# Kernel optimization log

Hardware: AMD Instinct MI355X
Metric: run time of the kernel (lower is better)

## Reference

```python
import jax, jax.numpy as jnp
import numpy as np

HEAD = 8
ATT = 32  # hard-coded att_num in the module
NEG_INF = -jnp.inf


def setup_inputs() -> dict:
    key0 = jax.random.key(0)
    ks = jax.random.split(key0, 12)
    B, N, Din, Dout = 8, 2048, 256, 256
    W = HEAD * ATT  # 256
    s_in = 1.0 / np.sqrt(Din)
    s_w = 1.0 / np.sqrt(W)
    return {
        "query": jax.random.normal(ks[0], (B, N, Din), jnp.float32),
        "key": jax.random.normal(ks[1], (B, N, Din), jnp.float32),
        "value": jax.random.normal(ks[2], (B, N, Din), jnp.float32),
        # torch.nn.Linear convention: W [out, in], y = x @ W.T + b
        "Wq": jax.random.normal(ks[3], (W, Din), jnp.float32) * s_in,
        "bq": jax.random.normal(ks[4], (W,), jnp.float32) * s_in,
        "Wk": jax.random.normal(ks[5], (W, Din), jnp.float32) * s_in,
        "bk": jax.random.normal(ks[6], (W,), jnp.float32) * s_in,
        "Wv": jax.random.normal(ks[7], (W, Din), jnp.float32) * s_in,
        "bv": jax.random.normal(ks[8], (W,), jnp.float32) * s_in,
        "Wo": jax.random.normal(ks[9], (Dout, W), jnp.float32) * s_w,
        "bo": jax.random.normal(ks[10], (Dout,), jnp.float32) * s_w,
    }


def _split_heads(x, b):
    # [b, n, head*att] -> view(b, n, head, att).permute(2,0,1,3) -> [head*b, n, att]
    n = x.shape[1]
    return x.reshape(b, n, HEAD, ATT).transpose(2, 0, 1, 3).reshape(HEAD * b, n, ATT)


def reference(query, key, value, Wq, bq, Wk, bk, Wv, bv, Wo, bo):
    b = query.shape[0]
    q = _split_heads(query @ Wq.T + bq, b)   # [head*b, nq, att]
    k = _split_heads(key @ Wk.T + bk, b)     # [head*b, nk, att]
    v = _split_heads(value @ Wv.T + bv, b)   # [head*b, nk, att]

    att = jnp.einsum('bmd,bnd->bmn', q, k)   # [head*b, nq, nk]
    nq, nk = att.shape[-2], att.shape[-1]
    causal = jnp.tril(jnp.ones((nq, nk), dtype=bool))
    att = jnp.where(causal, att, NEG_INF)
    att = jax.nn.softmax(att / jnp.sqrt(jnp.float32(ATT)), axis=-1)

    out = jnp.einsum('bmn,bnd->bmd', att, v)  # [head*b, nq, att]
    # view(head, b, nq, att).permute(1,2,0,3) -> [b, nq, head*att]
    out = out.reshape(HEAD, b, nq, ATT).transpose(1, 2, 0, 3).reshape(b, nq, HEAD * ATT)
    return out @ Wo.T + bo
```

## Files before the change

### kernel.cpp

```cpp
#include <hip/hip_runtime.h>
#include <hip/hip_bf16.h>
#include <stdint.h>

typedef __bf16 bf16_t;
typedef __bf16 bf16x4 __attribute__((ext_vector_type(4)));
typedef __bf16 bf16x8 __attribute__((ext_vector_type(8)));
typedef float f32x4 __attribute__((ext_vector_type(4)));
typedef __attribute__((address_space(3))) bf16_t* ldsp;

#define HEADS 8
#define ATTD 32
#define NBATCH 8
#define SEQ 2048
#define DIN 256
#define WDIM 256
#define MTOT (NBATCH*SEQ)
#define HBSZ ((size_t)MTOT*WDIM)
#define SCALE_L2E 0.25503322964704155f

#define EXP2R __builtin_amdgcn_exp2f

__device__ __forceinline__ uint32_t cvtpk(float a, float b) {
    uint32_t r;
    asm("v_cvt_pk_bf16_f32 %0, %1, %2" : "=v"(r) : "v"(a), "v"(b));
    return r;
}

template<int MODE>
__global__ __launch_bounds__(256) void gemm_kernel(
    const void* __restrict__ X0, const void* __restrict__ X1,
    const void* __restrict__ X2,
    const float* __restrict__ W0, const float* __restrict__ W1,
    const float* __restrict__ W2,
    const float* __restrict__ b0, const float* __restrict__ b1,
    const float* __restrict__ b2, void* __restrict__ outbase)
{
    __shared__ bf16_t As[128*64];
    __shared__ bf16_t Bs[128*64];

    const int tid = threadIdx.x;
    const int z   = blockIdx.z;
    const int m0  = blockIdx.y * 128;
    const int n0  = blockIdx.x * 128;
    const void*  Xin  = (z == 0) ? X0 : (z == 1) ? X1 : X2;
    const float* Wf   = (z == 0) ? W0 : (z == 1) ? W1 : W2;
    const float* bias = (z == 0) ? b0 : (z == 1) ? b1 : b2;

    const int wv = tid >> 6, ln = tid & 63, g = ln >> 4, l15 = ln & 15;
    const int wm = wv >> 1, wn = wv & 1;

    f32x4 acc[4][4];
#pragma unroll
    for (int i = 0; i < 4; ++i)
#pragma unroll
        for (int j = 0; j < 4; ++j) acc[i][j] = (f32x4){0.f,0.f,0.f,0.f};

    for (int kt = 0; kt < DIN/64; ++kt) {
        if (kt) __syncthreads();
#pragma unroll
        for (int iss = 0; iss < 4; ++iss) {
            int chunk = iss*256 + tid;
            int row = chunk >> 3, c8 = (chunk & 7) * 8;
            union { bf16_t h[8]; bf16x8 v; } av, bvv;
            if (MODE == 0) {
                const float* A = (const float*)Xin;
                float4 a0 = *(const float4*)(A + (size_t)(m0+row)*DIN + kt*64 + c8);
                float4 a1 = *(const float4*)(A + (size_t)(m0+row)*DIN + kt*64 + c8 + 4);
                av.h[0]=(bf16_t)a0.x; av.h[1]=(bf16_t)a0.y; av.h[2]=(bf16_t)a0.z; av.h[3]=(bf16_t)a0.w;
                av.h[4]=(bf16_t)a1.x; av.h[5]=(bf16_t)a1.y; av.h[6]=(bf16_t)a1.z; av.h[7]=(bf16_t)a1.w;
            } else {
                av.v = *(const bf16x8*)((const bf16_t*)Xin + (size_t)(m0+row)*DIN + kt*64 + c8);
            }
            float4 w0 = *(const float4*)(Wf + (size_t)(n0+row)*DIN + kt*64 + c8);
            float4 w1 = *(const float4*)(Wf + (size_t)(n0+row)*DIN + kt*64 + c8 + 4);
            bvv.h[0]=(bf16_t)w0.x; bvv.h[1]=(bf16_t)w0.y; bvv.h[2]=(bf16_t)w0.z; bvv.h[3]=(bf16_t)w0.w;
            bvv.h[4]=(bf16_t)w1.x; bvv.h[5]=(bf16_t)w1.y; bvv.h[6]=(bf16_t)w1.z; bvv.h[7]=(bf16_t)w1.w;
            *(bf16x8*)(As + chunk*8) = av.v;
            *(bf16x8*)(Bs + chunk*8) = bvv.v;
        }
        __syncthreads();
#pragma unroll
        for (int kk = 0; kk < 2; ++kk) {
            bf16x8 af[4], bfr[4];
#pragma unroll
            for (int i = 0; i < 4; ++i)
                af[i] = *(const bf16x8*)(As + (wm*64 + i*16 + l15)*64 + kk*32 + g*8);
#pragma unroll
            for (int j = 0; j < 4; ++j)
                bfr[j] = *(const bf16x8*)(Bs + (wn*64 + j*16 + l15)*64 + kk*32 + g*8);
#pragma unroll
            for (int i = 0; i < 4; ++i)
#pragma unroll
                for (int j = 0; j < 4; ++j)
                    acc[i][j] = __builtin_amdgcn_mfma_f32_16x16x32_bf16(
                        af[i], bfr[j], acc[i][j], 0, 0, 0);
        }
    }

    if (MODE == 0) {
        const int mrow   = m0 + wm*64 + g*4;
        const int ohbase = (n0 >> 5) + wn*2;
        bf16_t* out = (bf16_t*)outbase + (size_t)z * HBSZ;
        const float sc = (z == 0) ? SCALE_L2E : 1.0f;
#pragma unroll
        for (int j = 0; j < 4; ++j) {
            const int oh = ohbase + (j >> 1);
            const int ol = (j & 1)*16 + l15;
            bf16_t* p = out + ((size_t)oh*MTOT + mrow)*ATTD + ol;
            const float bb = bias[(oh << 5) | ol];
#pragma unroll
            for (int i = 0; i < 4; ++i)
#pragma unroll
                for (int r = 0; r < 4; ++r)
                    p[i*16*ATTD + r*ATTD] = (bf16_t)((acc[i][j][r] + bb) * sc);
        }
    } else {
        const int mrow = m0 + wm*64 + g*4;
        const int ocol = n0 + wn*64 + l15;
        float* out = (float*)outbase;
        float bb[4];
#pragma unroll
        for (int j = 0; j < 4; ++j) bb[j] = bias[ocol + j*16];
#pragma unroll
        for (int i = 0; i < 4; ++i) {
            float* p = out + (size_t)(mrow + i*16)*WDIM + ocol;
#pragma unroll
            for (int j = 0; j < 4; ++j)
#pragma unroll
                for (int r = 0; r < 4; ++r)
                    p[r*WDIM + j*16] = acc[i][j][r] + bb[j];
        }
    }
}

__global__ __launch_bounds__(512) void attn_kernel(
    const bf16_t* __restrict__ Qh, const bf16_t* __restrict__ Kh,
    const bf16_t* __restrict__ Vh, bf16_t* __restrict__ ATTo)
{
    __shared__ __align__(1024) bf16_t Ks[2][2][64*40];
    __shared__ __align__(1024) bf16_t Vsub[2][2][2048];

    const int qtx = blockIdx.x;
    const int bh  = blockIdx.y;
    const int hh = bh >> 3, bb = bh & 7;
    const int tid = threadIdx.x;
    const int wv = tid >> 6, ln = tid & 63, g = ln >> 4, l15 = ln & 15;
    const int grp = wv >> 2;
    const int wvi = wv & 3;
    const int t256 = tid & 255;

    const int kr = t256 >> 2, kc = (t256 & 3) * 8;
    const int vdst = ((kr >> 2) * 2 + ((t256 & 3) >> 1)) * 64 + (kr & 3) * 16 + (t256 & 1) * 8;
    const f32x4 zero4 = {0.f,0.f,0.f,0.f};
    const size_t bhs = (size_t)bh * SEQ;

    float* scr = (float*)&Ks[0][0][0];

    bf16x8 ones;
#pragma unroll
    for (int e = 0; e < 8; ++e) ones[e] = (bf16_t)1.0f;

    for (int half = 0; half < 2; ++half) {
        const int qt = half ? (31 - qtx) : qtx;
        const int n0 = qt * 64;
        const int nIter = (qt >> 1) + 1;
        const int q = n0 + wvi*16 + l15;
        const bf16x8 qfrag = *(const bf16x8*)(Qh + (bhs + q)*ATTD + g*8);
        f32x4 o0 = zero4, o1 = zero4, lsum = zero4;
        float m = -1e30f;

        {
            bf16x8 k0 = *(const bf16x8*)(Kh + (bhs + grp*64 + kr)*ATTD + kc);
            bf16x8 v0 = *(const bf16x8*)(Vh + (bhs + grp*64 + kr)*ATTD + kc);
            __syncthreads();
            *(bf16x8*)(&Ks[grp][0][kr*40 + kc]) = k0;
            *(bf16x8*)(&Vsub[grp][0][vdst]) = v0;
        }

        const bf16_t* kpref = Kh + (bhs + (grp+2)*64 + kr)*ATTD + kc;
        const bf16_t* vpref = Vh + (bhs + (grp+2)*64 + kr)*ATTD + kc;

        for (int t = 0; t < nIter; ++t) {
            const int cur = t & 1;
            const int myT = 2*t + grp;
            bf16x8 kreg = *(const bf16x8*)kpref; kpref += 128*ATTD;
            bf16x8 vreg = *(const bf16x8*)vpref; vpref += 128*ATTD;
            __syncthreads();

            if (myT <= qt) {
                f32x4 s[4];
#pragma unroll
                for (int c = 0; c < 4; ++c) {
                    bf16x8 kf = *(const bf16x8*)(&Ks[grp][cur][(c*16 + l15)*40 + g*8]);
                    s[c] = __builtin_amdgcn_mfma_f32_16x16x32_bf16(kf, qfrag, zero4, 0, 0, 0);
                }
                if (myT == qt) {
#pragma unroll
                    for (int c = 0; c < 4; ++c)
#pragma unroll
                        for (int r = 0; r < 4; ++r)
                            if (c*16 + g*4 + r > wvi*16 + l15) s[c][r] = -1e30f;
                }
                float t0 = fmaxf(fmaxf(s[0][0], s[0][1]), s[0][2]);
                float t1 = fmaxf(fmaxf(s[0][3], s[1][0]), s[1][1]);
                float t2 = fmaxf(fmaxf(s[1][2], s[1][3]), s[2][0]);
                float t3 = fmaxf(fmaxf(s[2][1], s[2][2]), s[2][3]);
                float t4 = fmaxf(fmaxf(s[3][0], s[3][1]), s[3][2]);
                float pmax = fmaxf(fmaxf(fmaxf(t0, t1), fmaxf(t2, t3)),
                                   fmaxf(t4, s[3][3]));
                pmax = fmaxf(pmax, __shfl_xor(pmax, 16));
                pmax = fmaxf(pmax, __shfl_xor(pmax, 32));
                if (!__all(pmax <= m)) {
                    const float mnew = fmaxf(m, pmax);
                    const float alpha = EXP2R(m - mnew);
                    m = mnew;
                    lsum[0] *= alpha;
#pragma unroll
                    for (int r = 0; r < 4; ++r) { o0[r] *= alpha; o1[r] *= alpha; }
                }
                union { uint32_t u[4]; bf16x8 v; } pb0, pb1;
                pb0.u[0] = cvtpk(EXP2R(s[0][0]-m), EXP2R(s[0][1]-m));
                pb0.u[1] = cvtpk(EXP2R(s[0][2]-m), EXP2R(s[0][3]-m));
                pb0.u[2] = cvtpk(EXP2R(s[1][0]-m), EXP2R(s[1][1]-m));
                pb0.u[3] = cvtpk(EXP2R(s[1][2]-m), EXP2R(s[1][3]-m));
                pb1.u[0] = cvtpk(EXP2R(s[2][0]-m), EXP2R(s[2][1]-m));
                pb1.u[1] = cvtpk(EXP2R(s[2][2]-m), EXP2R(s[2][3]-m));
                pb1.u[2] = cvtpk(EXP2R(s[3][0]-m), EXP2R(s[3][1]-m));
                pb1.u[3] = cvtpk(EXP2R(s[3][2]-m), EXP2R(s[3][3]-m));
                ldsp va = (ldsp)&Vsub[grp][cur][0] + g*128 + l15*4;
                bf16x4 t00, t01, t02, t03, t10, t11, t12, t13;
                asm volatile("ds_read_b64_tr_b16 %0, %1 offset:0"    : "=v"(t00) : "v"(va));
                asm volatile("ds_read_b64_tr_b16 %0, %1 offset:1024" : "=v"(t01) : "v"(va));
                asm volatile("ds_read_b64_tr_b16 %0, %1 offset:2048" : "=v"(t02) : "v"(va));
                asm volatile("ds_read_b64_tr_b16 %0, %1 offset:3072" : "=v"(t03) : "v"(va));
                asm volatile("ds_read_b64_tr_b16 %0, %1 offset:128"  : "=v"(t10) : "v"(va));
                asm volatile("ds_read_b64_tr_b16 %0, %1 offset:1152" : "=v"(t11) : "v"(va));
                asm volatile("ds_read_b64_tr_b16 %0, %1 offset:2176" : "=v"(t12) : "v"(va));
                asm volatile("ds_read_b64_tr_b16 %0, %1 offset:3200" : "=v"(t13) : "v"(va));
                asm volatile("s_waitcnt lgkmcnt(0)" ::: "memory");
                __builtin_amdgcn_sched_barrier(0);
                o0 = __builtin_amdgcn_mfma_f32_16x16x32_bf16(
                    __builtin_shufflevector(t00, t01, 0,1,2,3,4,5,6,7), pb0.v, o0, 0,0,0);
                o0 = __builtin_amdgcn_mfma_f32_16x16x32_bf16(
                    __builtin_shufflevector(t02, t03, 0,1,2,3,4,5,6,7), pb1.v, o0, 0,0,0);
                o1 = __builtin_amdgcn_mfma_f32_16x16x32_bf16(
                    __builtin_shufflevector(t10, t11, 0,1,2,3,4,5,6,7), pb0.v, o1, 0,0,0);
                o1 = __builtin_amdgcn_mfma_f32_16x16x32_bf16(
                    __builtin_shufflevector(t12, t13, 0,1,2,3,4,5,6,7), pb1.v, o1, 0,0,0);
                lsum = __builtin_amdgcn_mfma_f32_16x16x32_bf16(ones, pb0.v, lsum, 0,0,0);
                lsum = __builtin_amdgcn_mfma_f32_16x16x32_bf16(ones, pb1.v, lsum, 0,0,0);
            }

            *(bf16x8*)(&Ks[grp][cur^1][kr*40 + kc]) = kreg;
            *(bf16x8*)(&Vsub[grp][cur^1][vdst]) = vreg;
        }

        __syncthreads();
        const int sidx = (wvi*64 + ln)*10;
        if (grp == 1) {
            scr[sidx]   = m;
            scr[sidx+1] = lsum[0];
#pragma unroll
            for (int r = 0; r < 4; ++r) { scr[sidx+2+r] = o0[r]; scr[sidx+6+r] = o1[r]; }
        }
        __syncthreads();
        if (grp == 0) {
            const float mB = scr[sidx], lB = scr[sidx+1];
            const float mM = fmaxf(m, mB);
            const float aA = EXP2R(m - mM), aB = EXP2R(mB - mM);
            const float inv = 1.f / (lsum[0]*aA + lB*aB);
            union { bf16_t h[4]; uint2 u; } w0, w1;
#pragma unroll
            for (int r = 0; r < 4; ++r) {
                w0.h[r] = (bf16_t)((o0[r]*aA + scr[sidx+2+r]*aB) * inv);
                w1.h[r] = (bf16_t)((o1[r]*aA + scr[sidx+6+r]*aB) * inv);
            }
            const size_t base = ((size_t)bb*SEQ + q)*WDIM + hh*ATTD;
            *(uint2*)(ATTo + base + g*4)      = w0.u;
            *(uint2*)(ATTo + base + 16 + g*4) = w1.u;
        }
    }
}

extern "C" void kernel_launch(void* const* d_in, const int* in_sizes, int n_in,
                              void* d_out, int out_size, void* d_ws, size_t ws_size,
                              hipStream_t stream) {
    const float* q_in = (const float*)d_in[0];
    const float* k_in = (const float*)d_in[1];
    const float* v_in = (const float*)d_in[2];
    const float* Wq = (const float*)d_in[3];
    const float* bq = (const float*)d_in[4];
    const float* Wk = (const float*)d_in[5];
    const float* bk = (const float*)d_in[6];
    const float* Wv = (const float*)d_in[7];
    const float* bv = (const float*)d_in[8];
    const float* Wo = (const float*)d_in[9];
    const float* bo = (const float*)d_in[10];

    bf16_t* QKVh = (bf16_t*)d_ws;
    bf16_t* ATTo = QKVh + 3*HBSZ;

    gemm_kernel<0><<<dim3(2,128,3), 256, 0, stream>>>(
        q_in, k_in, v_in, Wq, Wk, Wv, bq, bk, bv, QKVh);
    attn_kernel<<<dim3(16,64), 512, 0, stream>>>(
        QKVh, QKVh + HBSZ, QKVh + 2*HBSZ, ATTo);
    gemm_kernel<1><<<dim3(2,128,1), 256, 0, stream>>>(
        ATTo, nullptr, nullptr, Wo, nullptr, nullptr, bo, nullptr, nullptr, d_out);
}
```

Baseline: 83.69 us.

## Retile projection GEMMs to 64x256 and remap attention block order

The projection GEMMs now give each block 64 rows and the full 256 output columns, so each activation tile is read from global memory only once, not once per column tile. Each of the four waves owns a 64-column slice. The attention grid is flattened to 1D with a custom mapping that places the 8 batches sharing a head and query tile in consecutive blocks, which should improve L2 locality or load balance. The cost is twice the weight staging per block: a 256x64 tile of W is converted from fp32 each k-step, and the larger B tile uses more LDS.

```diff
diff --git a/kernel.cpp b/kernel.cpp
--- a/kernel.cpp
+++ b/kernel.cpp
@@ -35,19 +35,17 @@
     const float* __restrict__ b0, const float* __restrict__ b1,
     const float* __restrict__ b2, void* __restrict__ outbase)
 {
-    __shared__ bf16_t As[128*64];
-    __shared__ bf16_t Bs[128*64];
+    __shared__ bf16_t As[64*64];
+    __shared__ bf16_t Bs[256*64];
 
     const int tid = threadIdx.x;
     const int z   = blockIdx.z;
-    const int m0  = blockIdx.y * 128;
-    const int n0  = blockIdx.x * 128;
+    const int m0  = blockIdx.y * 64;
     const void*  Xin  = (z == 0) ? X0 : (z == 1) ? X1 : X2;
     const float* Wf   = (z == 0) ? W0 : (z == 1) ? W1 : W2;
     const float* bias = (z == 0) ? b0 : (z == 1) ? b1 : b2;
 
     const int wv = tid >> 6, ln = tid & 63, g = ln >> 4, l15 = ln & 15;
-    const int wm = wv >> 1, wn = wv & 1;
 
     f32x4 acc[4][4];
 #pragma unroll
@@ -58,10 +56,10 @@
     for (int kt = 0; kt < DIN/64; ++kt) {
         if (kt) __syncthreads();
 #pragma unroll
-        for (int iss = 0; iss < 4; ++iss) {
+        for (int iss = 0; iss < 2; ++iss) {
             int chunk = iss*256 + tid;
             int row = chunk >> 3, c8 = (chunk & 7) * 8;
-            union { bf16_t h[8]; bf16x8 v; } av, bvv;
+            union { bf16_t h[8]; bf16x8 v; } av;
             if (MODE == 0) {
                 const float* A = (const float*)Xin;
                 float4 a0 = *(const float4*)(A + (size_t)(m0+row)*DIN + kt*64 + c8);
@@ -71,11 +69,17 @@
             } else {
                 av.v = *(const bf16x8*)((const bf16_t*)Xin + (size_t)(m0+row)*DIN + kt*64 + c8);
             }
-            float4 w0 = *(const float4*)(Wf + (size_t)(n0+row)*DIN + kt*64 + c8);
-            float4 w1 = *(const float4*)(Wf + (size_t)(n0+row)*DIN + kt*64 + c8 + 4);
+            *(bf16x8*)(As + chunk*8) = av.v;
+        }
+#pragma unroll
+        for (int iss = 0; iss < 8; ++iss) {
+            int chunk = iss*256 + tid;
+            int row = chunk >> 3, c8 = (chunk & 7) * 8;
+            union { bf16_t h[8]; bf16x8 v; } bvv;
+            float4 w0 = *(const float4*)(Wf + (size_t)row*DIN + kt*64 + c8);
+            float4 w1 = *(const float4*)(Wf + (size_t)row*DIN + kt*64 + c8 + 4);
             bvv.h[0]=(bf16_t)w0.x; bvv.h[1]=(bf16_t)w0.y; bvv.h[2]=(bf16_t)w0.z; bvv.h[3]=(bf16_t)w0.w;
             bvv.h[4]=(bf16_t)w1.x; bvv.h[5]=(bf16_t)w1.y; bvv.h[6]=(bf16_t)w1.z; bvv.h[7]=(bf16_t)w1.w;
-            *(bf16x8*)(As + chunk*8) = av.v;
             *(bf16x8*)(Bs + chunk*8) = bvv.v;
         }
         __syncthreads();
@@ -84,10 +88,10 @@
             bf16x8 af[4], bfr[4];
 #pragma unroll
             for (int i = 0; i < 4; ++i)
-                af[i] = *(const bf16x8*)(As + (wm*64 + i*16 + l15)*64 + kk*32 + g*8);
+                af[i] = *(const bf16x8*)(As + (i*16 + l15)*64 + kk*32 + g*8);
 #pragma unroll
             for (int j = 0; j < 4; ++j)
-                bfr[j] = *(const bf16x8*)(Bs + (wn*64 + j*16 + l15)*64 + kk*32 + g*8);
+                bfr[j] = *(const bf16x8*)(Bs + (wv*64 + j*16 + l15)*64 + kk*32 + g*8);
 #pragma unroll
             for (int i = 0; i < 4; ++i)
 #pragma unroll
@@ -98,13 +102,12 @@
     }
 
     if (MODE == 0) {
-        const int mrow   = m0 + wm*64 + g*4;
-        const int ohbase = (n0 >> 5) + wn*2;
+        const int mrow = m0 + g*4;
         bf16_t* out = (bf16_t*)outbase + (size_t)z * HBSZ;
         const float sc = (z == 0) ? SCALE_L2E : 1.0f;
 #pragma unroll
         for (int j = 0; j < 4; ++j) {
-            const int oh = ohbase + (j >> 1);
+            const int oh = wv*2 + (j >> 1);
             const int ol = (j & 1)*16 + l15;
             bf16_t* p = out + ((size_t)oh*MTOT + mrow)*ATTD + ol;
             const float bb = bias[(oh << 5) | ol];
@@ -115,8 +118,8 @@
                     p[i*16*ATTD + r*ATTD] = (bf16_t)((acc[i][j][r] + bb) * sc);
         }
     } else {
-        const int mrow = m0 + wm*64 + g*4;
-        const int ocol = n0 + wn*64 + l15;
+        const int mrow = m0 + g*4;
+        const int ocol = wv*64 + l15;
         float* out = (float*)outbase;
         float bb[4];
 #pragma unroll
@@ -140,8 +143,9 @@
     __shared__ __align__(1024) bf16_t Ks[2][2][64*40];
     __shared__ __align__(1024) bf16_t Vsub[2][2][2048];
 
-    const int qtx = blockIdx.x;
-    const int bh  = blockIdx.y;
+    const int id  = blockIdx.x;
+    const int qtx = (id >> 3) & 15;
+    const int bh  = ((id >> 7) << 3) | (id & 7);
     const int hh = bh >> 3, bb = bh & 7;
     const int tid = threadIdx.x;
     const int wv = tid >> 6, ln = tid & 63, g = ln >> 4, l15 = ln & 15;
@@ -300,10 +304,10 @@
     bf16_t* QKVh = (bf16_t*)d_ws;
     bf16_t* ATTo = QKVh + 3*HBSZ;
 
-    gemm_kernel<0><<<dim3(2,128,3), 256, 0, stream>>>(
+    gemm_kernel<0><<<dim3(1,256,3), 256, 0, stream>>>(
         q_in, k_in, v_in, Wq, Wk, Wv, bq, bk, bv, QKVh);
-    attn_kernel<<<dim3(16,64), 512, 0, stream>>>(
+    attn_kernel<<<dim3(1024), 512, 0, stream>>>(
         QKVh, QKVh + HBSZ, QKVh + 2*HBSZ, ATTo);
-    gemm_kernel<1><<<dim3(2,128,1), 256, 0, stream>>>(
+    gemm_kernel<1><<<dim3(1,256,1), 256, 0, stream>>>(
         ATTo, nullptr, nullptr, Wo, nullptr, nullptr, bo, nullptr, nullptr, d_out);
 }
```

After: 90.45 us. 8.1% more time.
